# Kernel tuning notes

Measured on AMD Instinct MI355X. Metric: run time of the kernel, lower is better.

The kernel has to match this reference:

```python
import jax, jax.numpy as jnp
import numpy as np

MODEL_DIM = 1024
NUM_HEADS = 16
K_DIM = MODEL_DIM // NUM_HEADS


def setup_inputs() -> dict:
    key = jax.random.key(0)
    k1, k2, k3 = jax.random.split(key, 3)
    x = jax.random.normal(k1, (4, 2048, MODEL_DIM), dtype=jnp.float32)
    # nn.Linear(model_dim, 3*model_dim, bias=False): store as [D, 3D] so y = x @ W
    wqkv = jax.random.normal(k2, (MODEL_DIM, 3 * MODEL_DIM), dtype=jnp.float32) * (MODEL_DIM ** -0.5)
    wo = jax.random.normal(k3, (MODEL_DIM, MODEL_DIM), dtype=jnp.float32) * (MODEL_DIM ** -0.5)
    return {"x": x, "wqkv": wqkv, "wo": wo}


def reference(x, wqkv, wo):
    B, L, D = x.shape
    H, K = NUM_HEADS, K_DIM
    qkv = jnp.einsum("bld,de->ble", x, wqkv)  # [B, L, 3D]
    q, k, v = jnp.split(qkv, 3, axis=-1)
    # Faithful to source: plain reshape (no transpose) into [B, H, L, K]
    qh = q.reshape(B, H, L, K)
    kh = k.reshape(B, H, L, K)
    vh = v.reshape(B, H, L, K)
    scores = jnp.einsum("bhlk,bhmk->bhlm", qh, kh) / jnp.sqrt(jnp.float32(K))
    # Faithful quirk: softmax over dim=1 (head axis), as in the source
    probs = jax.nn.softmax(scores, axis=1)
    attended = jnp.einsum("bhlm,bhmk->bhlk", probs, vh)  # [B, H, L, K]
    concatted = attended.transpose(0, 2, 1, 3).reshape(B, L, D)
    return jnp.einsum("bld,de->ble", concatted, wo)
```

## Files before the change

### kernel.cpp

```cpp
#include <hip/hip_runtime.h>
#include <hip/hip_bf16.h>
#include <stdint.h>

typedef __attribute__((ext_vector_type(8))) short short8;
typedef __attribute__((ext_vector_type(4))) float floatx4;

#define QSCALE 0.18033688f

__device__ __forceinline__ unsigned short f2bf(float f) {
    unsigned int u = __float_as_uint(f);
    u += 0x7fffu + ((u >> 16) & 1u);
    return (unsigned short)(u >> 16);
}
__device__ __forceinline__ unsigned int pack2bf(float a, float b) {
    __hip_bfloat162 h = __float22bfloat162_rn(make_float2(a, b));
    return *reinterpret_cast<unsigned int*>(&h);
}

__global__ __launch_bounds__(256) void cvt_bf16(const float* __restrict__ src,
                                                unsigned short* __restrict__ dst, int n8) {
    int i = blockIdx.x * 256 + threadIdx.x;
    if (i >= n8) return;
    const float4 a = ((const float4*)src)[2 * i];
    const float4 b = ((const float4*)src)[2 * i + 1];
    ushort4 lo, hi;
    lo.x = f2bf(a.x); lo.y = f2bf(a.y); lo.z = f2bf(a.z); lo.w = f2bf(a.w);
    hi.x = f2bf(b.x); hi.y = f2bf(b.y); hi.z = f2bf(b.z); hi.w = f2bf(b.w);
    ((ushort4*)dst)[2 * i] = lo;
    ((ushort4*)dst)[2 * i + 1] = hi;
}

__global__ __launch_bounds__(256) void tcvt(const float* __restrict__ src,
                                            unsigned short* __restrict__ dst, int R, int C) {
    __shared__ unsigned short t[64][72];
    const int tid = threadIdx.x;
    const int r0 = blockIdx.y * 64, c0 = blockIdx.x * 64;
    #pragma unroll
    for (int it = 0; it < 4; it++) {
        int idx = it * 256 + tid;
        int rr = idx >> 4, cc = (idx & 15) * 4;
        float4 v = *(const float4*)(src + (size_t)(r0 + rr) * C + c0 + cc);
        t[cc + 0][rr] = f2bf(v.x);
        t[cc + 1][rr] = f2bf(v.y);
        t[cc + 2][rr] = f2bf(v.z);
        t[cc + 3][rr] = f2bf(v.w);
    }
    __syncthreads();
    #pragma unroll
    for (int it = 0; it < 2; it++) {
        int idx = it * 256 + tid;
        int cc = idx >> 3, r8 = (idx & 7) * 8;
        short8 v = *(const short8*)&t[cc][r8];
        *(short8*)(dst + (size_t)(c0 + cc) * R + r0 + r8) = v;
    }
}

__global__ __launch_bounds__(256) void vtrans(const unsigned short* __restrict__ vb,
                                              unsigned short* __restrict__ vbt) {
    __shared__ unsigned short t[64][72];
    const int tid = threadIdx.x;
    const int bh = blockIdx.y, m0 = blockIdx.x * 64;
    const unsigned short* src = vb + ((size_t)bh * 2048 + m0) * 64;
    unsigned short* dst = vbt + ((size_t)bh << 17) + m0;
    union { short8 v; unsigned short u[8]; } tmp;
    #pragma unroll
    for (int it = 0; it < 2; it++) {
        int idx = it * 256 + tid;
        int m = idx >> 3, c8 = (idx & 7) * 8;
        tmp.v = *(const short8*)(src + (size_t)m * 64 + c8);
        #pragma unroll
        for (int j = 0; j < 8; j++) t[c8 + j][m] = tmp.u[j];
    }
    __syncthreads();
    #pragma unroll
    for (int it = 0; it < 2; it++) {
        int idx = it * 256 + tid;
        int k = idx >> 3, c8 = (idx & 7) * 8;
        short8 v = *(const short8*)&t[k][c8];
        *(short8*)(dst + (size_t)k * 2048 + c8) = v;
    }
}

__global__ __launch_bounds__(256) void qkv_gemm(
    const unsigned short* __restrict__ A, const unsigned short* __restrict__ Bt,
    unsigned short* __restrict__ qb, unsigned short* __restrict__ kb,
    unsigned short* __restrict__ vb)
{
    __shared__ __align__(16) unsigned short As[128 * 32];
    __shared__ __align__(16) unsigned short Bs[128 * 32];
    const int tid = threadIdx.x, wave = tid >> 6, lane = tid & 63;
    const int quad = lane >> 4, lr = lane & 15;
    const int wr = wave >> 1, wc = wave & 1;
    const int bm = blockIdx.y * 128, bn = blockIdx.x * 128;
    const int srow = wave * 32 + (lane >> 2);
    const int sblk = lane & 3;

    floatx4 acc[4][4];
    #pragma unroll
    for (int i = 0; i < 4; i++)
        #pragma unroll
        for (int j = 0; j < 4; j++) acc[i][j] = (floatx4)0.0f;

    for (int k0 = 0; k0 < 1024; k0 += 32) {
        #pragma unroll
        for (int t = 0; t < 2; t++) {
            int r = srow + t * 16;
            short8 va = *(const short8*)(A  + (size_t)(bm + r) * 1024 + k0 + sblk * 8);
            short8 vw = *(const short8*)(Bt + (size_t)(bn + r) * 1024 + k0 + sblk * 8);
            *(short8*)&As[r * 32 + sblk * 8] = va;
            *(short8*)&Bs[r * 32 + sblk * 8] = vw;
        }
        __syncthreads();
        short8 af[4], bfr[4];
        #pragma unroll
        for (int i = 0; i < 4; i++)
            af[i] = *(const short8*)&As[(wr * 64 + i * 16 + lr) * 32 + quad * 8];
        #pragma unroll
        for (int j = 0; j < 4; j++)
            bfr[j] = *(const short8*)&Bs[(wc * 64 + j * 16 + lr) * 32 + quad * 8];
        #pragma unroll
        for (int i = 0; i < 4; i++)
            #pragma unroll
            for (int j = 0; j < 4; j++)
                acc[i][j] = __builtin_amdgcn_mfma_f32_16x16x32_bf16(af[i], bfr[j], acc[i][j], 0, 0, 0);
        __syncthreads();
    }

    const int part = bn >> 10;
    unsigned short* __restrict__ dstb = (part == 0) ? qb : ((part == 1) ? kb : vb);
    const float sc = (part == 0) ? QSCALE : 1.0f;
    const int dbase = bn & 1023;
    #pragma unroll
    for (int i = 0; i < 4; i++)
        #pragma unroll
        for (int j = 0; j < 4; j++)
            #pragma unroll
            for (int r = 0; r < 4; r++) {
                int row = bm + wr * 64 + i * 16 + quad * 4 + r;
                int d   = dbase + wc * 64 + j * 16 + lr;
                int b = row >> 11, l = row & 2047;
                int flat = (l << 10) | d;
                int h = flat >> 17;
                int rem = flat & 131071;
                int l2 = rem >> 6, kk = rem & 63;
                dstb[((size_t)(b * 16 + h) * 2048 + l2) * 64 + kk] = f2bf(acc[i][j][r] * sc);
            }
}

__global__ __launch_bounds__(256) void out_gemm(
    const unsigned short* __restrict__ A, const unsigned short* __restrict__ Bt,
    float* __restrict__ C)
{
    __shared__ __align__(16) unsigned short As[128 * 32];
    __shared__ __align__(16) unsigned short Bs[128 * 32];
    const int tid = threadIdx.x, wave = tid >> 6, lane = tid & 63;
    const int quad = lane >> 4, lr = lane & 15;
    const int wr = wave >> 1, wc = wave & 1;
    const int bm = blockIdx.y * 128, bn = blockIdx.x * 128;
    const int srow = wave * 32 + (lane >> 2);
    const int sblk = lane & 3;

    floatx4 acc[4][4];
    #pragma unroll
    for (int i = 0; i < 4; i++)
        #pragma unroll
        for (int j = 0; j < 4; j++) acc[i][j] = (floatx4)0.0f;

    for (int k0 = 0; k0 < 1024; k0 += 32) {
        #pragma unroll
        for (int t = 0; t < 2; t++) {
            int r = srow + t * 16;
            short8 va = *(const short8*)(A  + (size_t)(bm + r) * 1024 + k0 + sblk * 8);
            short8 vw = *(const short8*)(Bt + (size_t)(bn + r) * 1024 + k0 + sblk * 8);
            *(short8*)&As[r * 32 + sblk * 8] = va;
            *(short8*)&Bs[r * 32 + sblk * 8] = vw;
        }
        __syncthreads();
        short8 af[4], bfr[4];
        #pragma unroll
        for (int i = 0; i < 4; i++)
            af[i] = *(const short8*)&As[(wr * 64 + i * 16 + lr) * 32 + quad * 8];
        #pragma unroll
        for (int j = 0; j < 4; j++)
            bfr[j] = *(const short8*)&Bs[(wc * 64 + j * 16 + lr) * 32 + quad * 8];
        #pragma unroll
        for (int i = 0; i < 4; i++)
            #pragma unroll
            for (int j = 0; j < 4; j++)
                acc[i][j] = __builtin_amdgcn_mfma_f32_16x16x32_bf16(af[i], bfr[j], acc[i][j], 0, 0, 0);
        __syncthreads();
    }
    #pragma unroll
    for (int i = 0; i < 4; i++)
        #pragma unroll
        for (int j = 0; j < 4; j++)
            #pragma unroll
            for (int r = 0; r < 4; r++) {
                int row = bm + wr * 64 + i * 16 + quad * 4 + r;
                int col = bn + wc * 64 + j * 16 + lr;
                C[(size_t)row * 1024 + col] = acc[i][j][r];
            }
}

__global__ __launch_bounds__(256, 4) void attn_denom(
    const unsigned short* __restrict__ qb, const unsigned short* __restrict__ kb,
    unsigned short* __restrict__ drpT)
{
    __shared__ __align__(16) unsigned short Qs[64 * 64];
    __shared__ __align__(16) unsigned short Ks[64 * 64];
    const int tid = threadIdx.x, wave = tid >> 6, lane = tid & 63;
    const int quad = lane >> 4, lr = lane & 15;
    const int M0 = blockIdx.x * 64, L0 = blockIdx.y * 64, b = blockIdx.z;
    const int srow = tid >> 3, sblk = tid & 7;
    const int sphys = (sblk ^ (srow & 7)) * 8;

    floatx4 e[4];
    #pragma unroll
    for (int i = 0; i < 4; i++) e[i] = (floatx4)0.0f;

    {
        const size_t hb = ((size_t)(b * 16)) << 17;
        short8 q0 = *(const short8*)(qb + hb + (size_t)(L0 + srow) * 64 + sblk * 8);
        short8 q1 = *(const short8*)(qb + hb + (size_t)(L0 + srow + 32) * 64 + sblk * 8);
        short8 k0 = *(const short8*)(kb + hb + (size_t)(M0 + srow) * 64 + sblk * 8);
        short8 k1 = *(const short8*)(kb + hb + (size_t)(M0 + srow + 32) * 64 + sblk * 8);
        *(short8*)&Qs[srow * 64 + sphys] = q0;
        *(short8*)&Qs[(srow + 32) * 64 + sphys] = q1;
        *(short8*)&Ks[srow * 64 + sphys] = k0;
        *(short8*)&Ks[(srow + 32) * 64 + sphys] = k1;
    }
    __syncthreads();

    for (int h = 0; h < 16; h++) {
        short8 qn0, qn1, kn0, kn1;
        if (h < 15) {
            const size_t hb = ((size_t)(b * 16 + h + 1)) << 17;
            qn0 = *(const short8*)(qb + hb + (size_t)(L0 + srow) * 64 + sblk * 8);
            qn1 = *(const short8*)(qb + hb + (size_t)(L0 + srow + 32) * 64 + sblk * 8);
            kn0 = *(const short8*)(kb + hb + (size_t)(M0 + srow) * 64 + sblk * 8);
            kn1 = *(const short8*)(kb + hb + (size_t)(M0 + srow + 32) * 64 + sblk * 8);
        }
        const int rq = wave * 16 + lr;
        short8 qf0 = *(const short8*)&Qs[rq * 64 + ((quad) ^ (lr & 7)) * 8];
        short8 qf1 = *(const short8*)&Qs[rq * 64 + ((4 + quad) ^ (lr & 7)) * 8];
        #pragma unroll
        for (int mt = 0; mt < 4; mt++) {
            const int rk = mt * 16 + lr;
            short8 kf0 = *(const short8*)&Ks[rk * 64 + ((quad) ^ (lr & 7)) * 8];
            short8 kf1 = *(const short8*)&Ks[rk * 64 + ((4 + quad) ^ (lr & 7)) * 8];
            floatx4 s = (floatx4)0.0f;
            s = __builtin_amdgcn_mfma_f32_16x16x32_bf16(kf0, qf0, s, 0, 0, 0);
            s = __builtin_amdgcn_mfma_f32_16x16x32_bf16(kf1, qf1, s, 0, 0, 0);
            e[mt][0] += __builtin_amdgcn_exp2f(s[0]);
            e[mt][1] += __builtin_amdgcn_exp2f(s[1]);
            e[mt][2] += __builtin_amdgcn_exp2f(s[2]);
            e[mt][3] += __builtin_amdgcn_exp2f(s[3]);
        }
        __syncthreads();
        if (h < 15) {
            *(short8*)&Qs[srow * 64 + sphys] = qn0;
            *(short8*)&Qs[(srow + 32) * 64 + sphys] = qn1;
            *(short8*)&Ks[srow * 64 + sphys] = kn0;
            *(short8*)&Ks[(srow + 32) * 64 + sphys] = kn1;
            __syncthreads();
        }
    }
    #pragma unroll
    for (int mt = 0; mt < 4; mt++) {
        float r0 = __builtin_amdgcn_rcpf(e[mt][0]);
        float r1 = __builtin_amdgcn_rcpf(e[mt][1]);
        float r2 = __builtin_amdgcn_rcpf(e[mt][2]);
        float r3 = __builtin_amdgcn_rcpf(e[mt][3]);
        uint2 o;
        o.x = pack2bf(r0, r1);
        o.y = pack2bf(r2, r3);
        int mtg = (M0 >> 4) + mt;
        int ltg = (L0 >> 4) + wave;
        *(uint2*)(drpT + ((((size_t)b * 128 + mtg) * 128 + ltg) << 8) + lane * 4) = o;
    }
}

__global__ __launch_bounds__(256, 4) void attn_pv(
    const unsigned short* __restrict__ qb, const unsigned short* __restrict__ kb,
    const unsigned short* __restrict__ vbt, const unsigned short* __restrict__ drpT,
    unsigned short* __restrict__ cb)
{
    __shared__ __align__(16) unsigned short Ks[2][64 * 64];
    __shared__ __align__(16) unsigned short Ps[128 * 64];
    const int tid = threadIdx.x, wave = tid >> 6, lane = tid & 63;
    const int quad = lane >> 4, lr = lane & 15;
    const int L0 = blockIdx.x * 128, h = blockIdx.y, b = blockIdx.z;
    const size_t head = (size_t)(b * 16 + h);
    const unsigned short* qbase = qb + (head << 17);
    const unsigned short* kbase = kb + (head << 17);
    const unsigned short* vtb   = vbt + (head << 17);
    const int krow = tid >> 3, ksb = tid & 7;
    const int kphys = (ksb ^ (krow & 7)) * 8;
    const int e7 = lr & 7;

    short8 qf[2][2];
    #pragma unroll
    for (int j = 0; j < 2; j++) {
        const unsigned short* qr = qbase + (size_t)(L0 + wave * 32 + j * 16 + lr) * 64;
        qf[j][0] = *(const short8*)(qr + quad * 8);
        qf[j][1] = *(const short8*)(qr + 32 + quad * 8);
    }

    floatx4 oacc[2][4];
    #pragma unroll
    for (int i = 0; i < 2; i++)
        #pragma unroll
        for (int j = 0; j < 4; j++) oacc[i][j] = (floatx4)0.0f;

    {
        short8 a = *(const short8*)(kbase + (size_t)krow * 64 + ksb * 8);
        short8 c = *(const short8*)(kbase + (size_t)(krow + 32) * 64 + ksb * 8);
        *(short8*)&Ks[0][krow * 64 + kphys] = a;
        *(short8*)&Ks[0][(krow + 32) * 64 + kphys] = c;
    }
    __syncthreads();

    for (int t = 0; t < 32; t++) {
        const int M0 = t * 64;
        const unsigned short* ksrc = &Ks[t & 1][0];
        short8 nka, nkc;
        if (t < 31) {
            nka = *(const short8*)(kbase + (size_t)(M0 + 64 + krow) * 64 + ksb * 8);
            nkc = *(const short8*)(kbase + (size_t)(M0 + 64 + krow + 32) * 64 + ksb * 8);
        }
        #pragma unroll
        for (int mt = 0; mt < 4; mt++) {
            const int rk = mt * 16 + lr;
            short8 kf0 = *(const short8*)&ksrc[rk * 64 + (quad ^ e7) * 8];
            short8 kf1 = *(const short8*)&ksrc[rk * 64 + ((4 + quad) ^ e7) * 8];
            const int mtg = (M0 >> 4) + mt;
            #pragma unroll
            for (int j = 0; j < 2; j++) {
                const int ltg = (L0 >> 4) + wave * 2 + j;
                uint2 du = *(const uint2*)(drpT + ((((size_t)b * 128 + mtg) * 128 + ltg) << 8) + lane * 4);
                floatx4 s = (floatx4)0.0f;
                s = __builtin_amdgcn_mfma_f32_16x16x32_bf16(kf0, qf[j][0], s, 0, 0, 0);
                s = __builtin_amdgcn_mfma_f32_16x16x32_bf16(kf1, qf[j][1], s, 0, 0, 0);
                float r0 = __uint_as_float(du.x << 16);
                float r1 = __uint_as_float(du.x & 0xffff0000u);
                float r2 = __uint_as_float(du.y << 16);
                float r3 = __uint_as_float(du.y & 0xffff0000u);
                float p0 = __builtin_amdgcn_exp2f(s[0]) * r0;
                float p1 = __builtin_amdgcn_exp2f(s[1]) * r1;
                float p2 = __builtin_amdgcn_exp2f(s[2]) * r2;
                float p3 = __builtin_amdgcn_exp2f(s[3]) * r3;
                uint2 o;
                o.x = pack2bf(p0, p1);
                o.y = pack2bf(p2, p3);
                const int l_loc = wave * 32 + j * 16 + lr;
                const int lb16 = mt * 2 + (quad >> 1);
                const int phys16 = lb16 ^ e7;
                *(uint2*)&Ps[l_loc * 64 + phys16 * 8 + (quad & 1) * 4] = o;
            }
        }
        #pragma unroll
        for (int f = 0; f < 2; f++) {
            short8 pf[2];
            #pragma unroll
            for (int i2 = 0; i2 < 2; i2++) {
                const int lrow = wave * 32 + i2 * 16 + lr;
                const int phys16 = (f * 4 + quad) ^ e7;
                pf[i2] = *(const short8*)&Ps[lrow * 64 + phys16 * 8];
            }
            #pragma unroll
            for (int j2 = 0; j2 < 4; j2++) {
                const int nrow = j2 * 16 + lr;
                short8 vf = *(const short8*)(vtb + (size_t)nrow * 2048 + M0 + f * 32 + quad * 8);
                #pragma unroll
                for (int i2 = 0; i2 < 2; i2++)
                    oacc[i2][j2] = __builtin_amdgcn_mfma_f32_16x16x32_bf16(pf[i2], vf, oacc[i2][j2], 0, 0, 0);
            }
        }
        if (t < 31) {
            unsigned short* kdst = &Ks[(t + 1) & 1][0];
            *(short8*)&kdst[krow * 64 + kphys] = nka;
            *(short8*)&kdst[(krow + 32) * 64 + kphys] = nkc;
            __syncthreads();
        }
    }
    #pragma unroll
    for (int i2 = 0; i2 < 2; i2++)
        #pragma unroll
        for (int j2 = 0; j2 < 4; j2++)
            #pragma unroll
            for (int r = 0; r < 4; r++) {
                int row = L0 + wave * 32 + i2 * 16 + quad * 4 + r;
                int col = h * 64 + j2 * 16 + lr;
                cb[(size_t)(b * 2048 + row) * 1024 + col] = f2bf(oacc[i2][j2][r]);
            }
}

extern "C" void kernel_launch(void* const* d_in, const int* in_sizes, int n_in,
                              void* d_out, int out_size, void* d_ws, size_t ws_size,
                              hipStream_t stream) {
    const float* x    = (const float*)d_in[0];
    const float* wqkv = (const float*)d_in[1];
    const float* wo   = (const float*)d_in[2];
    float* out = (float*)d_out;

    unsigned short* W = (unsigned short*)d_ws;
    unsigned short* qb   = W;
    unsigned short* kb   = W + 8388608;
    unsigned short* vbt  = W + 16777216;
    unsigned short* drpT = W + 25165824;
    unsigned short* cb   = W + 41943040;
    unsigned short* xb    = drpT;
    unsigned short* wqkvT = drpT + 8388608;
    unsigned short* vb    = cb;
    unsigned short* woT   = drpT;

    cvt_bf16  <<<4096, 256, 0, stream>>>(x, xb, 1048576);
    tcvt      <<<dim3(48, 16), 256, 0, stream>>>(wqkv, wqkvT, 1024, 3072);
    qkv_gemm  <<<dim3(24, 64), 256, 0, stream>>>(xb, wqkvT, qb, kb, vb);
    vtrans    <<<dim3(32, 64), 256, 0, stream>>>(vb, vbt);
    attn_denom<<<dim3(32, 32, 4), 256, 0, stream>>>(qb, kb, drpT);
    attn_pv   <<<dim3(16, 16, 4), 256, 0, stream>>>(qb, kb, vbt, drpT, cb);
    tcvt      <<<dim3(16, 16), 256, 0, stream>>>(wo, woT, 1024, 1024);
    out_gemm  <<<dim3(8, 64), 256, 0, stream>>>(cb, woT, out);
}
```

Measured before the change: 428.1 us.

## Halve attn_pv row tile, software-pipeline QK/exp and PV stages, prefetch denominators

The attn_pv kernel now processes 64 query rows per block (16 per wave) instead of 128, which doubles the grid to 2048 blocks and frees registers for occupancy. The loop is skewed so that iteration t computes the probability tile for K-tile t while running the PV MFMAs on the tile from t-1, using a double-buffered per-wave P buffer in shared memory. The reciprocal-denominator values are prefetched into registers one tile ahead. The cost is that each block re-reads K and V for half as many rows, doubling K/V traffic, plus one extra loop iteration for the pipeline drain.

```diff
diff --git a/kernel.cpp b/kernel.cpp
--- a/kernel.cpp
+++ b/kernel.cpp
@@ -286,10 +286,10 @@
     unsigned short* __restrict__ cb)
 {
     __shared__ __align__(16) unsigned short Ks[2][64 * 64];
-    __shared__ __align__(16) unsigned short Ps[128 * 64];
+    __shared__ __align__(16) unsigned short Ps[2][4][16 * 64];
     const int tid = threadIdx.x, wave = tid >> 6, lane = tid & 63;
     const int quad = lane >> 4, lr = lane & 15;
-    const int L0 = blockIdx.x * 128, h = blockIdx.y, b = blockIdx.z;
+    const int L0 = blockIdx.x * 64, h = blockIdx.y, b = blockIdx.z;
     const size_t head = (size_t)(b * 16 + h);
     const unsigned short* qbase = qb + (head << 17);
     const unsigned short* kbase = kb + (head << 17);
@@ -297,54 +297,62 @@
     const int krow = tid >> 3, ksb = tid & 7;
     const int kphys = (ksb ^ (krow & 7)) * 8;
     const int e7 = lr & 7;
-
-    short8 qf[2][2];
-    #pragma unroll
-    for (int j = 0; j < 2; j++) {
-        const unsigned short* qr = qbase + (size_t)(L0 + wave * 32 + j * 16 + lr) * 64;
-        qf[j][0] = *(const short8*)(qr + quad * 8);
-        qf[j][1] = *(const short8*)(qr + 32 + quad * 8);
-    }
-
-    floatx4 oacc[2][4];
-    #pragma unroll
-    for (int i = 0; i < 2; i++)
-        #pragma unroll
-        for (int j = 0; j < 4; j++) oacc[i][j] = (floatx4)0.0f;
-
+    const int ltg = (L0 >> 4) + wave;
+    const size_t drp_lt_base = (((size_t)b * 128) * 128 + ltg) << 8;
+
+    short8 qf0, qf1;
+    {
+        const unsigned short* qr = qbase + (size_t)(L0 + wave * 16 + lr) * 64;
+        qf0 = *(const short8*)(qr + quad * 8);
+        qf1 = *(const short8*)(qr + 32 + quad * 8);
+    }
+
+    floatx4 oacc[4];
+    #pragma unroll
+    for (int j = 0; j < 4; j++) oacc[j] = (floatx4)0.0f;
+
+    uint2 dureg[4];
     {
         short8 a = *(const short8*)(kbase + (size_t)krow * 64 + ksb * 8);
         short8 c = *(const short8*)(kbase + (size_t)(krow + 32) * 64 + ksb * 8);
         *(short8*)&Ks[0][krow * 64 + kphys] = a;
         *(short8*)&Ks[0][(krow + 32) * 64 + kphys] = c;
+        #pragma unroll
+        for (int mt = 0; mt < 4; mt++)
+            dureg[mt] = *(const uint2*)(drpT + drp_lt_base + ((size_t)mt << 15) + lane * 4);
     }
     __syncthreads();
 
-    for (int t = 0; t < 32; t++) {
-        const int M0 = t * 64;
-        const unsigned short* ksrc = &Ks[t & 1][0];
+    for (int t = 0; t <= 32; t++) {
         short8 nka, nkc;
         if (t < 31) {
-            nka = *(const short8*)(kbase + (size_t)(M0 + 64 + krow) * 64 + ksb * 8);
-            nkc = *(const short8*)(kbase + (size_t)(M0 + 64 + krow + 32) * 64 + ksb * 8);
-        }
-        #pragma unroll
-        for (int mt = 0; mt < 4; mt++) {
-            const int rk = mt * 16 + lr;
-            short8 kf0 = *(const short8*)&ksrc[rk * 64 + (quad ^ e7) * 8];
-            short8 kf1 = *(const short8*)&ksrc[rk * 64 + ((4 + quad) ^ e7) * 8];
-            const int mtg = (M0 >> 4) + mt;
-            #pragma unroll
-            for (int j = 0; j < 2; j++) {
-                const int ltg = (L0 >> 4) + wave * 2 + j;
-                uint2 du = *(const uint2*)(drpT + ((((size_t)b * 128 + mtg) * 128 + ltg) << 8) + lane * 4);
+            nka = *(const short8*)(kbase + (size_t)((t + 1) * 64 + krow) * 64 + ksb * 8);
+            nkc = *(const short8*)(kbase + (size_t)((t + 1) * 64 + krow + 32) * 64 + ksb * 8);
+        }
+        if (t < 32) {
+            uint2 duse[4];
+            #pragma unroll
+            for (int mt = 0; mt < 4; mt++) duse[mt] = dureg[mt];
+            if (t < 31) {
+                #pragma unroll
+                for (int mt = 0; mt < 4; mt++)
+                    dureg[mt] = *(const uint2*)(drpT + drp_lt_base +
+                                 (((size_t)((t + 1) * 4 + mt)) << 15) + lane * 4);
+            }
+            const unsigned short* ksrc = &Ks[t & 1][0];
+            unsigned short* pl = &Ps[t & 1][wave][0];
+            #pragma unroll
+            for (int mt = 0; mt < 4; mt++) {
+                const int rk = mt * 16 + lr;
+                short8 kf0 = *(const short8*)&ksrc[rk * 64 + (quad ^ e7) * 8];
+                short8 kf1 = *(const short8*)&ksrc[rk * 64 + ((4 + quad) ^ e7) * 8];
                 floatx4 s = (floatx4)0.0f;
-                s = __builtin_amdgcn_mfma_f32_16x16x32_bf16(kf0, qf[j][0], s, 0, 0, 0);
-                s = __builtin_amdgcn_mfma_f32_16x16x32_bf16(kf1, qf[j][1], s, 0, 0, 0);
-                float r0 = __uint_as_float(du.x << 16);
-                float r1 = __uint_as_float(du.x & 0xffff0000u);
-                float r2 = __uint_as_float(du.y << 16);
-                float r3 = __uint_as_float(du.y & 0xffff0000u);
+                s = __builtin_amdgcn_mfma_f32_16x16x32_bf16(kf0, qf0, s, 0, 0, 0);
+                s = __builtin_amdgcn_mfma_f32_16x16x32_bf16(kf1, qf1, s, 0, 0, 0);
+                float r0 = __uint_as_float(duse[mt].x << 16);
+                float r1 = __uint_as_float(duse[mt].x & 0xffff0000u);
+                float r2 = __uint_as_float(duse[mt].y << 16);
+                float r3 = __uint_as_float(duse[mt].y & 0xffff0000u);
                 float p0 = __builtin_amdgcn_exp2f(s[0]) * r0;
                 float p1 = __builtin_amdgcn_exp2f(s[1]) * r1;
                 float p2 = __builtin_amdgcn_exp2f(s[2]) * r2;
@@ -352,28 +360,21 @@
                 uint2 o;
                 o.x = pack2bf(p0, p1);
                 o.y = pack2bf(p2, p3);
-                const int l_loc = wave * 32 + j * 16 + lr;
-                const int lb16 = mt * 2 + (quad >> 1);
-                const int phys16 = lb16 ^ e7;
-                *(uint2*)&Ps[l_loc * 64 + phys16 * 8 + (quad & 1) * 4] = o;
+                const int b16 = mt * 2 + (quad >> 1);
+                *(uint2*)&pl[lr * 64 + (b16 ^ e7) * 8 + (quad & 1) * 4] = o;
             }
         }
-        #pragma unroll
-        for (int f = 0; f < 2; f++) {
-            short8 pf[2];
-            #pragma unroll
-            for (int i2 = 0; i2 < 2; i2++) {
-                const int lrow = wave * 32 + i2 * 16 + lr;
-                const int phys16 = (f * 4 + quad) ^ e7;
-                pf[i2] = *(const short8*)&Ps[lrow * 64 + phys16 * 8];
-            }
-            #pragma unroll
-            for (int j2 = 0; j2 < 4; j2++) {
-                const int nrow = j2 * 16 + lr;
-                short8 vf = *(const short8*)(vtb + (size_t)nrow * 2048 + M0 + f * 32 + quad * 8);
+        if (t > 0) {
+            const int Mp = (t - 1) * 64;
+            const unsigned short* pl = &Ps[(t - 1) & 1][wave][0];
+            #pragma unroll
+            for (int f = 0; f < 2; f++) {
+                short8 pf = *(const short8*)&pl[lr * 64 + ((f * 4 + quad) ^ e7) * 8];
                 #pragma unroll
-                for (int i2 = 0; i2 < 2; i2++)
-                    oacc[i2][j2] = __builtin_amdgcn_mfma_f32_16x16x32_bf16(pf[i2], vf, oacc[i2][j2], 0, 0, 0);
+                for (int j2 = 0; j2 < 4; j2++) {
+                    short8 vf = *(const short8*)(vtb + (size_t)(j2 * 16 + lr) * 2048 + Mp + f * 32 + quad * 8);
+                    oacc[j2] = __builtin_amdgcn_mfma_f32_16x16x32_bf16(pf, vf, oacc[j2], 0, 0, 0);
+                }
             }
         }
         if (t < 31) {
@@ -384,15 +385,13 @@
         }
     }
     #pragma unroll
-    for (int i2 = 0; i2 < 2; i2++)
-        #pragma unroll
-        for (int j2 = 0; j2 < 4; j2++)
-            #pragma unroll
-            for (int r = 0; r < 4; r++) {
-                int row = L0 + wave * 32 + i2 * 16 + quad * 4 + r;
-                int col = h * 64 + j2 * 16 + lr;
-                cb[(size_t)(b * 2048 + row) * 1024 + col] = f2bf(oacc[i2][j2][r]);
-            }
+    for (int j2 = 0; j2 < 4; j2++)
+        #pragma unroll
+        for (int r = 0; r < 4; r++) {
+            int row = L0 + wave * 16 + quad * 4 + r;
+            int col = h * 64 + j2 * 16 + lr;
+            cb[(size_t)(b * 2048 + row) * 1024 + col] = f2bf(oacc[j2][r]);
+        }
 }
 
 extern "C" void kernel_launch(void* const* d_in, const int* in_sizes, int n_in,
@@ -419,7 +418,7 @@
     qkv_gemm  <<<dim3(24, 64), 256, 0, stream>>>(xb, wqkvT, qb, kb, vb);
     vtrans    <<<dim3(32, 64), 256, 0, stream>>>(vb, vbt);
     attn_denom<<<dim3(32, 32, 4), 256, 0, stream>>>(qb, kb, drpT);
-    attn_pv   <<<dim3(16, 16, 4), 256, 0, stream>>>(qb, kb, vbt, drpT, cb);
+    attn_pv   <<<dim3(32, 16, 4), 256, 0, stream>>>(qb, kb, vbt, drpT, cb);
     tcvt      <<<dim3(16, 16), 256, 0, stream>>>(wo, woT, 1024, 1024);
     out_gemm  <<<dim3(8, 64), 256, 0, stream>>>(cb, woT, out);
 }
```

Result: slower. 536.2 us (+25.2%).

## Use direct global-to-LDS loads in GEMMs and prefetch V and softmax-denominator tiles in attention

Applied to the files above, without the earlier changes.

The QKV and output GEMMs now stage tiles with global_load_lds, which moves data straight from global memory into shared memory without passing through registers. The attention PV kernel loads all V fragments at the start of each tile, so they are in flight during the score computation. It also double-buffers the per-tile reciprocal (drpT) values in registers, fetching the next tile's values after the current exp step. The goal is to hide global memory latency, at the cost of more registers under a launch bound of 4 blocks per CU, and the async LDS path relies on correct implicit wait handling at the barrier.

```diff
diff --git a/kernel.cpp b/kernel.cpp
--- a/kernel.cpp
+++ b/kernel.cpp
@@ -15,6 +15,12 @@
 __device__ __forceinline__ unsigned int pack2bf(float a, float b) {
     __hip_bfloat162 h = __float22bfloat162_rn(make_float2(a, b));
     return *reinterpret_cast<unsigned int*>(&h);
+}
+
+__device__ __forceinline__ void async16(const void* g, void* l) {
+    __builtin_amdgcn_global_load_lds(
+        (const __attribute__((address_space(1))) unsigned int*)g,
+        (__attribute__((address_space(3))) unsigned int*)l, 16, 0, 0);
 }
 
 __global__ __launch_bounds__(256) void cvt_bf16(const float* __restrict__ src,
@@ -92,8 +98,7 @@
     const int quad = lane >> 4, lr = lane & 15;
     const int wr = wave >> 1, wc = wave & 1;
     const int bm = blockIdx.y * 128, bn = blockIdx.x * 128;
-    const int srow = wave * 32 + (lane >> 2);
-    const int sblk = lane & 3;
+    const int lrow = lane >> 2, lcol = (lane & 3) * 8;
 
     floatx4 acc[4][4];
     #pragma unroll
@@ -104,11 +109,10 @@
     for (int k0 = 0; k0 < 1024; k0 += 32) {
         #pragma unroll
         for (int t = 0; t < 2; t++) {
-            int r = srow + t * 16;
-            short8 va = *(const short8*)(A  + (size_t)(bm + r) * 1024 + k0 + sblk * 8);
-            short8 vw = *(const short8*)(Bt + (size_t)(bn + r) * 1024 + k0 + sblk * 8);
-            *(short8*)&As[r * 32 + sblk * 8] = va;
-            *(short8*)&Bs[r * 32 + sblk * 8] = vw;
+            const int rbase = wave * 32 + t * 16;
+            const int r = rbase + lrow;
+            async16(A  + (size_t)(bm + r) * 1024 + k0 + lcol, &As[rbase * 32]);
+            async16(Bt + (size_t)(bn + r) * 1024 + k0 + lcol, &Bs[rbase * 32]);
         }
         __syncthreads();
         short8 af[4], bfr[4];
@@ -157,8 +161,7 @@
     const int quad = lane >> 4, lr = lane & 15;
     const int wr = wave >> 1, wc = wave & 1;
     const int bm = blockIdx.y * 128, bn = blockIdx.x * 128;
-    const int srow = wave * 32 + (lane >> 2);
-    const int sblk = lane & 3;
+    const int lrow = lane >> 2, lcol = (lane & 3) * 8;
 
     floatx4 acc[4][4];
     #pragma unroll
@@ -169,11 +172,10 @@
     for (int k0 = 0; k0 < 1024; k0 += 32) {
         #pragma unroll
         for (int t = 0; t < 2; t++) {
-            int r = srow + t * 16;
-            short8 va = *(const short8*)(A  + (size_t)(bm + r) * 1024 + k0 + sblk * 8);
-            short8 vw = *(const short8*)(Bt + (size_t)(bn + r) * 1024 + k0 + sblk * 8);
-            *(short8*)&As[r * 32 + sblk * 8] = va;
-            *(short8*)&Bs[r * 32 + sblk * 8] = vw;
+            const int rbase = wave * 32 + t * 16;
+            const int r = rbase + lrow;
+            async16(A  + (size_t)(bm + r) * 1024 + k0 + lcol, &As[rbase * 32]);
+            async16(Bt + (size_t)(bn + r) * 1024 + k0 + lcol, &Bs[rbase * 32]);
         }
         __syncthreads();
         short8 af[4], bfr[4];
@@ -296,7 +298,8 @@
     const unsigned short* vtb   = vbt + (head << 17);
     const int krow = tid >> 3, ksb = tid & 7;
     const int kphys = (ksb ^ (krow & 7)) * 8;
-    const int e7 = lr & 7;
+    const int e7 = lr & 15 & 7;
+    const unsigned short* dbase = drpT + (((size_t)b * 128 * 128 + ((L0 >> 4) + wave * 2)) << 8) + lane * 4;
 
     short8 qf[2][2];
     #pragma unroll
@@ -312,32 +315,43 @@
         #pragma unroll
         for (int j = 0; j < 4; j++) oacc[i][j] = (floatx4)0.0f;
 
+    uint2 dunext[4][2];
     {
         short8 a = *(const short8*)(kbase + (size_t)krow * 64 + ksb * 8);
         short8 c = *(const short8*)(kbase + (size_t)(krow + 32) * 64 + ksb * 8);
         *(short8*)&Ks[0][krow * 64 + kphys] = a;
         *(short8*)&Ks[0][(krow + 32) * 64 + kphys] = c;
+        #pragma unroll
+        for (int mt = 0; mt < 4; mt++)
+            #pragma unroll
+            for (int j = 0; j < 2; j++)
+                dunext[mt][j] = *(const uint2*)(dbase + ((size_t)mt << 15) + (j << 8));
     }
     __syncthreads();
 
     for (int t = 0; t < 32; t++) {
         const int M0 = t * 64;
-        const unsigned short* ksrc = &Ks[t & 1][0];
         short8 nka, nkc;
         if (t < 31) {
             nka = *(const short8*)(kbase + (size_t)(M0 + 64 + krow) * 64 + ksb * 8);
             nkc = *(const short8*)(kbase + (size_t)(M0 + 64 + krow + 32) * 64 + ksb * 8);
         }
+        short8 vfr[2][4];
+        #pragma unroll
+        for (int f = 0; f < 2; f++)
+            #pragma unroll
+            for (int j2 = 0; j2 < 4; j2++)
+                vfr[f][j2] = *(const short8*)(vtb + (size_t)(j2 * 16 + lr) * 2048 + M0 + f * 32 + quad * 8);
+
+        const unsigned short* ksrc = &Ks[t & 1][0];
         #pragma unroll
         for (int mt = 0; mt < 4; mt++) {
             const int rk = mt * 16 + lr;
             short8 kf0 = *(const short8*)&ksrc[rk * 64 + (quad ^ e7) * 8];
             short8 kf1 = *(const short8*)&ksrc[rk * 64 + ((4 + quad) ^ e7) * 8];
-            const int mtg = (M0 >> 4) + mt;
             #pragma unroll
             for (int j = 0; j < 2; j++) {
-                const int ltg = (L0 >> 4) + wave * 2 + j;
-                uint2 du = *(const uint2*)(drpT + ((((size_t)b * 128 + mtg) * 128 + ltg) << 8) + lane * 4);
+                uint2 du = dunext[mt][j];
                 floatx4 s = (floatx4)0.0f;
                 s = __builtin_amdgcn_mfma_f32_16x16x32_bf16(kf0, qf[j][0], s, 0, 0, 0);
                 s = __builtin_amdgcn_mfma_f32_16x16x32_bf16(kf1, qf[j][1], s, 0, 0, 0);
@@ -354,9 +368,15 @@
                 o.y = pack2bf(p2, p3);
                 const int l_loc = wave * 32 + j * 16 + lr;
                 const int lb16 = mt * 2 + (quad >> 1);
-                const int phys16 = lb16 ^ e7;
-                *(uint2*)&Ps[l_loc * 64 + phys16 * 8 + (quad & 1) * 4] = o;
+                *(uint2*)&Ps[l_loc * 64 + (lb16 ^ e7) * 8 + (quad & 1) * 4] = o;
             }
+        }
+        if (t < 31) {
+            #pragma unroll
+            for (int mt = 0; mt < 4; mt++)
+                #pragma unroll
+                for (int j = 0; j < 2; j++)
+                    dunext[mt][j] = *(const uint2*)(dbase + (((size_t)((t + 1) * 4 + mt)) << 15) + (j << 8));
         }
         #pragma unroll
         for (int f = 0; f < 2; f++) {
@@ -364,17 +384,13 @@
             #pragma unroll
             for (int i2 = 0; i2 < 2; i2++) {
                 const int lrow = wave * 32 + i2 * 16 + lr;
-                const int phys16 = (f * 4 + quad) ^ e7;
-                pf[i2] = *(const short8*)&Ps[lrow * 64 + phys16 * 8];
+                pf[i2] = *(const short8*)&Ps[lrow * 64 + ((f * 4 + quad) ^ e7) * 8];
             }
             #pragma unroll
-            for (int j2 = 0; j2 < 4; j2++) {
-                const int nrow = j2 * 16 + lr;
-                short8 vf = *(const short8*)(vtb + (size_t)nrow * 2048 + M0 + f * 32 + quad * 8);
+            for (int j2 = 0; j2 < 4; j2++)
                 #pragma unroll
                 for (int i2 = 0; i2 < 2; i2++)
-                    oacc[i2][j2] = __builtin_amdgcn_mfma_f32_16x16x32_bf16(pf[i2], vf, oacc[i2][j2], 0, 0, 0);
-            }
+                    oacc[i2][j2] = __builtin_amdgcn_mfma_f32_16x16x32_bf16(pf[i2], vfr[f][j2], oacc[i2][j2], 0, 0, 0);
         }
         if (t < 31) {
             unsigned short* kdst = &Ks[(t + 1) & 1][0];
```

Result: no change. 427.2 us (-0.2%).
